# Kernel optimization log

Measured on AMD Instinct MI355X. Metric: run time of the kernel, lower is better.

## Reference

```python
import jax, jax.numpy as jnp
import numpy as np

D_MODEL = 1024
NUM_HEADS = 16
D_K = D_MODEL // NUM_HEADS


def setup_inputs() -> dict:
    key = jax.random.key(0)
    k1, k2, k3, k4, k5 = jax.random.split(key, 5)
    x = jax.random.normal(k1, (2, 2048, D_MODEL), dtype=jnp.float32)
    s = 1.0 / np.sqrt(D_MODEL)
    W_q = jax.random.normal(k2, (D_MODEL, D_MODEL), dtype=jnp.float32) * s
    W_k = jax.random.normal(k3, (D_MODEL, D_MODEL), dtype=jnp.float32) * s
    W_v = jax.random.normal(k4, (D_MODEL, D_MODEL), dtype=jnp.float32) * s
    W_o = jax.random.normal(k5, (D_MODEL, D_MODEL), dtype=jnp.float32) * s
    return {"x": x, "W_q": W_q, "W_k": W_k, "W_v": W_v, "W_o": W_o}


def reference(x, W_q, W_k, W_v, W_o):
    B, S, _ = x.shape
    # projections (nn.Linear: y = x @ W.T); split heads -> (B, H, S, d_k)
    def split_heads(y):
        return y.reshape(B, S, NUM_HEADS, D_K).transpose(0, 2, 1, 3)
    Q = split_heads(x @ W_q.T)
    K = split_heads(x @ W_k.T)
    V = split_heads(x @ W_v.T)
    scale = 1.0 / jnp.sqrt(jnp.asarray(D_K, dtype=x.dtype))
    scores = jnp.einsum("bhqd,bhkd->bhqk", Q, K) * scale  # (B,H,S,S)
    causal = jnp.triu(jnp.ones((S, S), dtype=bool), k=1)
    scores = jnp.where(causal, -jnp.inf, scores)
    attn = jax.nn.softmax(scores, axis=-1)
    out = jnp.einsum("bhqk,bhkd->bhqd", attn, V)
    out = out.transpose(0, 2, 1, 3).reshape(B, S, D_MODEL)
    return out @ W_o.T
```

## Files before the change

### kernel.cpp

```cpp
#include <hip/hip_runtime.h>
#include <hip/hip_bf16.h>

typedef __bf16 bf16x8 __attribute__((ext_vector_type(8)));
typedef float f32x4 __attribute__((ext_vector_type(4)));
typedef float f32x16 __attribute__((ext_vector_type(16)));
typedef unsigned short ushort_t;
typedef unsigned int uint2v __attribute__((ext_vector_type(2)));

#define DEVI __device__ __forceinline__

static constexpr int KDIM = 1024;
static constexpr int SEQ  = 2048;
static constexpr size_t TEN = 4194304;

DEVI ushort_t f2bf(float f) {
  union { float f; unsigned u; } a; a.f = f;
  unsigned u = a.u;
  return (ushort_t)((u + 0x7FFFu + ((u >> 16) & 1u)) >> 16);
}

DEVI unsigned cvtpk(float lo, float hi) {
  unsigned r;
  asm("v_cvt_pk_bf16_f32 %0, %1, %2" : "=v"(r) : "v"(lo), "v"(hi));
  return r;
}

DEVI uint2v plswap(unsigned a, unsigned b) {
  return __builtin_amdgcn_permlane32_swap(a, b, 0, 0);
}
DEVI float swap_max(float x) {
  union { float f; unsigned u; } a; a.f = x;
  const uint2v r = plswap(a.u, a.u);
  union { unsigned u; float f; } p0, p1; p0.u = r[0]; p1.u = r[1];
  return fmaxf(p0.f, p1.f);
}
DEVI float swap_sum(float x) {
  union { float f; unsigned u; } a; a.f = x;
  const uint2v r = plswap(a.u, a.u);
  union { unsigned u; float f; } p0, p1; p0.u = r[0]; p1.u = r[1];
  return p0.f + p1.f;
}

DEVI void gload16(const ushort_t* g, ushort_t* l) {
  __builtin_amdgcn_global_load_lds(
      (const __attribute__((address_space(1))) void*)g,
      (__attribute__((address_space(3))) void*)l,
      16, 0, 0);
}

__global__ void cast_all(const float* __restrict__ x,
                         const float* __restrict__ w0, const float* __restrict__ w1,
                         const float* __restrict__ w2, const float* __restrict__ w3,
                         ushort_t* __restrict__ xb, ushort_t* __restrict__ wb) {
  const int i = blockIdx.x * 256 + threadIdx.x;
  float4 v; ushort_t* dst; int idx;
  if (i < (1 << 20)) {
    v = ((const float4*)x)[i]; dst = xb; idx = i;
  } else {
    const int j = i - (1 << 20);
    const int which = j >> 18;
    const float* w = which == 0 ? w0 : which == 1 ? w1 : which == 2 ? w2 : w3;
    v = ((const float4*)w)[j & 262143]; dst = wb; idx = j;
  }
  ushort4 o;
  o.x = f2bf(v.x); o.y = f2bf(v.y); o.z = f2bf(v.z); o.w = f2bf(v.w);
  ((ushort4*)dst)[idx] = o;
}

template<int MODE>
__global__ __launch_bounds__(256, 3) void gemm128(const ushort_t* __restrict__ A,
                                                  const ushort_t* __restrict__ Bm,
                                                  ushort_t* __restrict__ qfo,
                                                  ushort_t* __restrict__ kfo,
                                                  ushort_t* __restrict__ vfo,
                                                  float* __restrict__ ofp) {
  __shared__ ushort_t smA[128 * 64];
  __shared__ ushort_t smB[128 * 64];
  const int tid = threadIdx.x;
  const int w = tid >> 6, l = tid & 63;
  const int lg = l >> 4, ll = l & 15;
  const int lr = l >> 3, lc = (l & 7) * 8;
  const int m0 = blockIdx.y * 128, n0 = blockIdx.x * 128;
  const int wm = (w >> 1) * 64, wn = (w & 1) * 64;

  f32x4 acc[4][4];
#pragma unroll
  for (int i = 0; i < 4; ++i)
#pragma unroll
    for (int j = 0; j < 4; ++j) acc[i][j] = f32x4{0.f, 0.f, 0.f, 0.f};

  for (int k0 = 0; k0 < KDIM; k0 += 64) {
    __syncthreads();
#pragma unroll
    for (int i = 0; i < 4; ++i) {
      const int ci = w * 4 + i;
      gload16(A  + (size_t)(m0 + ci * 8 + lr) * KDIM + k0 + lc, smA + ci * 512);
      gload16(Bm + (size_t)(n0 + ci * 8 + lr) * KDIM + k0 + lc, smB + ci * 512);
    }
    __syncthreads();
#pragma unroll
    for (int ks = 0; ks < 2; ++ks) {
      bf16x8 af[4], bfr[4];
#pragma unroll
      for (int t = 0; t < 4; ++t) {
        af[t]  = *(const bf16x8*)(smA + (wm + t * 16 + ll) * 64 + ks * 32 + lg * 8);
        bfr[t] = *(const bf16x8*)(smB + (wn + t * 16 + ll) * 64 + ks * 32 + lg * 8);
      }
      __builtin_amdgcn_s_setprio(1);
#pragma unroll
      for (int i = 0; i < 4; ++i)
#pragma unroll
        for (int j = 0; j < 4; ++j)
          acc[i][j] = __builtin_amdgcn_mfma_f32_16x16x32_bf16(af[i], bfr[j], acc[i][j], 0, 0, 0);
      __builtin_amdgcn_s_setprio(0);
    }
  }

#pragma unroll
  for (int i = 0; i < 4; ++i) {
#pragma unroll
    for (int j = 0; j < 4; ++j) {
      const int gm0 = m0 + wm + i * 16 + 4 * lg;
      const int gn = n0 + wn + j * 16 + ll;
      if (MODE == 0) {
        const int which = gn >> 10, nn = gn & 1023;
        const int h = nn >> 6, d = nn & 63;
        const int b = gm0 >> 11, s0 = gm0 & 2047;
        const size_t bh = (size_t)(b * 16 + h);
        if (which == 0) {
          const int ks = d >> 4, hiv = (d >> 3) & 1, j7 = d & 7;
#pragma unroll
          for (int r = 0; r < 4; ++r) {
            const int s = s0 + r;
            qfo[((bh * 64 + (s >> 5)) * 4 + ks) * 512 + (hiv * 32 + (s & 31)) * 8 + j7] =
                f2bf(acc[i][j][r]);
          }
        } else if (which == 1) {
          const int ks = d >> 4, hiv = (d >> 3) & 1, j7 = d & 7;
#pragma unroll
          for (int r = 0; r < 4; ++r) {
            const int s = s0 + r;
            kfo[((bh * 32 + (s >> 6)) * 8 + ((s >> 5) & 1) * 4 + ks) * 512 +
                (hiv * 32 + (s & 31)) * 8 + j7] = f2bf(acc[i][j][r]);
          }
        } else {
          const size_t base = ((bh * 32 + (s0 >> 6)) * 8 + (d >> 5) * 4 + ((s0 >> 4) & 3)) * 512 +
                              (((s0 >> 3) & 1) * 32 + (d & 31)) * 8 + (s0 & 7);
          const unsigned u0 = cvtpk(acc[i][j][0], acc[i][j][1]);
          const unsigned u1 = cvtpk(acc[i][j][2], acc[i][j][3]);
          *(uint2v*)(vfo + base) = uint2v{u0, u1};
        }
      } else {
#pragma unroll
        for (int r = 0; r < 4; ++r)
          ofp[(size_t)(gm0 + r) * 1024 + gn] = acc[i][j][r];
      }
    }
  }
}

__global__ __launch_bounds__(256, 2) void attn_fwd(const ushort_t* __restrict__ Qf,
                                                   const ushort_t* __restrict__ Kf,
                                                   const ushort_t* __restrict__ Vf,
                                                   ushort_t* __restrict__ ao) {
  const int tid = threadIdx.x;
  const int w = tid >> 6, l = tid & 63;
  const int l31 = l & 31, hi = l >> 5;
  const int bh = blockIdx.y;
  const int qx = ((bh >> 4) & 1) ? (15 - (int)blockIdx.x) : (int)blockIdx.x;
  const int q0 = qx * 128;
  const int q = q0 + w * 32 + l31;

  const ushort_t* Qw = Qf + ((size_t)bh * 64 + (q0 >> 5) + w) * 4 * 512 + l * 8;
  const ushort_t* Kb = Kf + (size_t)bh * 32 * 8 * 512 + l * 8;
  const ushort_t* Vb = Vf + (size_t)bh * 32 * 8 * 512 + l * 8;

  bf16x8 qf[4];
#pragma unroll
  for (int ks = 0; ks < 4; ++ks)
    qf[ks] = *(const bf16x8*)(Qw + ks * 512);

  f32x16 oT[2];
#pragma unroll
  for (int dh = 0; dh < 2; ++dh)
#pragma unroll
    for (int r = 0; r < 16; ++r) oT[dh][r] = 0.f;
  float mi = -3.0e38f, li = 0.f;

  const float SCL2 = 0.18033688011112042f;
  const int myNkt = (q0 + 32 * w + 31) / 64 + 1;

  bf16x8 kf[8];
#pragma unroll
  for (int f = 0; f < 8; ++f) kf[f] = *(const bf16x8*)(Kb + f * 512);

  for (int kt = 0; kt < myNkt; ++kt) {
    const ushort_t* Vt_ = Vb + (size_t)kt * 8 * 512;
    bf16x8 vf[8];
#pragma unroll
    for (int f = 0; f < 8; ++f) vf[f] = *(const bf16x8*)(Vt_ + f * 512);

    f32x16 sc[2];
#pragma unroll
    for (int h2 = 0; h2 < 2; ++h2)
#pragma unroll
      for (int r = 0; r < 16; ++r) sc[h2][r] = 0.f;
    __builtin_amdgcn_s_setprio(1);
#pragma unroll
    for (int h2 = 0; h2 < 2; ++h2)
#pragma unroll
      for (int ks = 0; ks < 4; ++ks)
        sc[h2] = __builtin_amdgcn_mfma_f32_32x32x16_bf16(kf[h2 * 4 + ks], qf[ks], sc[h2], 0, 0, 0);
    __builtin_amdgcn_s_setprio(0);

    const bool more = (kt + 1 < myNkt);
    bf16x8 kfn[8];
    if (more) {
      const ushort_t* Kt_ = Kb + (size_t)(kt + 1) * 8 * 512;
#pragma unroll
      for (int f = 0; f < 8; ++f) kfn[f] = *(const bf16x8*)(Kt_ + f * 512);
    }

    if (kt == myNkt - 1) {
      const int thr0 = q - kt * 64 - 4 * hi;
#pragma unroll
      for (int r = 0; r < 16; ++r) {
        const int cr = (r & 3) + 8 * (r >> 2);
        if (cr > thr0)      sc[0][r] = -3.0e38f;
        if (cr > thr0 - 32) sc[1][r] = -3.0e38f;
      }
    }

    float t8[8];
#pragma unroll
    for (int r = 0; r < 8; ++r)
      t8[r] = fmaxf(fmaxf(sc[0][r], sc[0][r + 8]), fmaxf(sc[1][r], sc[1][r + 8]));
    float mx = fmaxf(fmaxf(fmaxf(t8[0], t8[1]), fmaxf(t8[2], t8[3])),
                     fmaxf(fmaxf(t8[4], t8[5]), fmaxf(t8[6], t8[7])));
    mx = swap_max(mx);

    if (!__all(mx <= mi + 44.0f)) {
      const float mnew = fmaxf(mi, mx);
      const float al = __builtin_amdgcn_exp2f((mi - mnew) * SCL2);
      li *= al;
#pragma unroll
      for (int dh = 0; dh < 2; ++dh)
#pragma unroll
        for (int r = 0; r < 16; ++r) oT[dh][r] *= al;
      mi = mnew;
    }

    const float ms = mi * SCL2;
#pragma unroll
    for (int h2 = 0; h2 < 2; ++h2)
#pragma unroll
      for (int r = 0; r < 16; ++r)
        sc[h2][r] = __builtin_amdgcn_exp2f(__builtin_fmaf(sc[h2][r], SCL2, -ms));
    float s8[8];
#pragma unroll
    for (int r = 0; r < 8; ++r)
      s8[r] = (sc[0][r] + sc[0][r + 8]) + (sc[1][r] + sc[1][r + 8]);
    float sum = ((s8[0] + s8[1]) + (s8[2] + s8[3])) + ((s8[4] + s8[5]) + (s8[6] + s8[7]));
    li += swap_sum(sum);

    bf16x8 pf[4];
#pragma unroll
    for (int m = 0; m < 4; ++m) {
      const int H = m >> 1, base = (m & 1) * 8;
      const unsigned a0 = cvtpk(sc[H][base + 0], sc[H][base + 1]);
      const unsigned a1 = cvtpk(sc[H][base + 2], sc[H][base + 3]);
      const unsigned a2 = cvtpk(sc[H][base + 4], sc[H][base + 5]);
      const unsigned a3 = cvtpk(sc[H][base + 6], sc[H][base + 7]);
      const uint2v r02 = plswap(a0, a2);
      const uint2v r13 = plswap(a1, a3);
      union { unsigned u[4]; bf16x8 v; } cv;
      cv.u[0] = r02[0]; cv.u[1] = r13[0]; cv.u[2] = r02[1]; cv.u[3] = r13[1];
      pf[m] = cv.v;
    }

    __builtin_amdgcn_s_setprio(1);
#pragma unroll
    for (int dh = 0; dh < 2; ++dh)
#pragma unroll
      for (int m = 0; m < 4; ++m)
        oT[dh] = __builtin_amdgcn_mfma_f32_32x32x16_bf16(vf[dh * 4 + m], pf[m], oT[dh], 0, 0, 0);
    __builtin_amdgcn_s_setprio(0);

    if (more) {
#pragma unroll
      for (int f = 0; f < 8; ++f) kf[f] = kfn[f];
    }
  }

  const float inv = 1.f / li;
  const int b = bh >> 4, h = bh & 15;
  ushort_t* orow = ao + ((size_t)b * 2048 + q) * 1024 + h * 64;
#pragma unroll
  for (int dh = 0; dh < 2; ++dh)
#pragma unroll
    for (int rg = 0; rg < 4; ++rg) {
      const unsigned u0 = cvtpk(oT[dh][4 * rg + 0] * inv, oT[dh][4 * rg + 1] * inv);
      const unsigned u1 = cvtpk(oT[dh][4 * rg + 2] * inv, oT[dh][4 * rg + 3] * inv);
      *(uint2v*)(orow + dh * 32 + hi * 4 + rg * 8) = uint2v{u0, u1};
    }
}

extern "C" void kernel_launch(void* const* d_in, const int* in_sizes, int n_in,
                              void* d_out, int out_size, void* d_ws, size_t ws_size,
                              hipStream_t stream) {
  (void)in_sizes; (void)n_in; (void)out_size; (void)ws_size;
  const float* x  = (const float*)d_in[0];
  const float* wq = (const float*)d_in[1];
  const float* wk = (const float*)d_in[2];
  const float* wv = (const float*)d_in[3];
  const float* wo = (const float*)d_in[4];

  char* ws = (char*)d_ws;
  ushort_t* xb  = (ushort_t*)ws;
  ushort_t* wb  = (ushort_t*)(ws + (8u  << 20));
  ushort_t* qf  = (ushort_t*)(ws + (16u << 20));
  ushort_t* kf  = (ushort_t*)(ws + (24u << 20));
  ushort_t* vf  = (ushort_t*)(ws + (40u << 20));
  ushort_t* ao  = xb;
  float* out = (float*)d_out;

  cast_all<<<8192, 256, 0, stream>>>(x, wq, wk, wv, wo, xb, wb);
  gemm128<0><<<dim3(24, 32), 256, 0, stream>>>(xb, wb, qf, kf, vf, nullptr);
  attn_fwd  <<<dim3(16, 32), 256, 0, stream>>>(qf, kf, vf, ao);
  gemm128<1><<<dim3(8, 32), 256, 0, stream>>>(ao, wb + 3 * 1048576, nullptr, nullptr, nullptr, out);
}
```

Measured before the change: 176.6 us.

## Replace QKV projection GEMM with 256x256-tile, 8-wave, double-buffered pipelined kernel

The QKV projection now uses a dedicated kernel with 256x256 output tiles and 512 threads. It double-buffers LDS in half-K chunks with asynchronous global-to-LDS loads and an XOR swizzle to avoid bank conflicts, and interleaves staging with the MFMA phases using vmcnt waits and barriers. Blocks are remapped so that consecutive tiles spread across XCDs. The goal is more data reuse per tile and hidden memory latency, at the cost of a grid of only 192 blocks, which is under one wave on 256 CUs.

After: 174.5 us. No clear change (-1.2%).

```diff
diff --git a/kernel.cpp b/kernel.cpp
--- a/kernel.cpp
+++ b/kernel.cpp
@@ -67,13 +67,140 @@
   ((ushort4*)dst)[idx] = o;
 }
 
-template<int MODE>
-__global__ __launch_bounds__(256, 3) void gemm128(const ushort_t* __restrict__ A,
-                                                  const ushort_t* __restrict__ Bm,
-                                                  ushort_t* __restrict__ qfo,
-                                                  ushort_t* __restrict__ kfo,
-                                                  ushort_t* __restrict__ vfo,
-                                                  float* __restrict__ ofp) {
+DEVI void stage_half(const ushort_t* __restrict__ G, int rowbase, int kcol,
+                     ushort_t* lbase, int tid) {
+#pragma unroll
+  for (int rd = 0; rd < 2; ++rd) {
+    const int row = rd * 128 + (tid >> 2), cg = tid & 3;
+    const int gcol = kcol + ((cg ^ ((row >> 1) & 3)) << 3);
+    gload16(G + (size_t)(rowbase + row) * 1024 + gcol, lbase + row * 32 + cg * 8);
+  }
+}
+
+__global__ __launch_bounds__(512, 2) void gemm256_qkv(const ushort_t* __restrict__ A,
+                                                      const ushort_t* __restrict__ Bm,
+                                                      ushort_t* __restrict__ qfo,
+                                                      ushort_t* __restrict__ kfo,
+                                                      ushort_t* __restrict__ vfo) {
+  __shared__ ushort_t sm[2][2][2][8192];
+  const int tid = threadIdx.x;
+  const int wid = tid >> 6, l = tid & 63;
+  const int wm = wid >> 2, wn = wid & 3;
+  const int lg = l >> 4, ll = l & 15;
+  const int orig = blockIdx.x;
+  const int wg = (orig & 7) * 24 + (orig >> 3);
+  const int bx = wg % 12, by = wg / 12;
+  const int m0 = by * 256, n0 = bx * 256;
+
+  f32x4 acc[8][4];
+#pragma unroll
+  for (int i = 0; i < 8; ++i)
+#pragma unroll
+    for (int j = 0; j < 4; ++j) acc[i][j] = f32x4{0.f, 0.f, 0.f, 0.f};
+
+#define STG(T, MAT, KH) do { if ((T) < 16) \
+    stage_half((MAT) ? Bm : A, (MAT) ? n0 : m0, (T) * 64 + (KH) * 32, \
+               &sm[(T) & 1][MAT][KH][0], tid); } while (0)
+#define BARX do { asm volatile("" ::: "memory"); __builtin_amdgcn_s_barrier(); \
+                  asm volatile("" ::: "memory"); } while (0)
+#define PHASE(P, KH, MH, STG_STMT, WAIT_STMT) do {                              \
+    bf16x8 af_[4], bf_[4];                                                      \
+    _Pragma("unroll")                                                           \
+    for (int mr = 0; mr < 4; ++mr) {                                            \
+      const int ra = wm * 128 + ((MH) * 4 + mr) * 16 + ll;                      \
+      af_[mr] = *(const bf16x8*)&sm[P][0][KH][ra * 32 + ((lg ^ ((ra >> 1) & 3)) << 3)]; \
+    }                                                                           \
+    _Pragma("unroll")                                                           \
+    for (int nr = 0; nr < 4; ++nr) {                                            \
+      const int rb = wn * 64 + nr * 16 + ll;                                    \
+      bf_[nr] = *(const bf16x8*)&sm[P][1][KH][rb * 32 + ((lg ^ ((rb >> 1) & 3)) << 3)]; \
+    }                                                                           \
+    STG_STMT;                                                                   \
+    BARX;                                                                       \
+    __builtin_amdgcn_s_setprio(1);                                              \
+    _Pragma("unroll")                                                           \
+    for (int mr = 0; mr < 4; ++mr)                                              \
+      _Pragma("unroll")                                                         \
+      for (int nr = 0; nr < 4; ++nr)                                            \
+        acc[(MH) * 4 + mr][nr] = __builtin_amdgcn_mfma_f32_16x16x32_bf16(       \
+            af_[mr], bf_[nr], acc[(MH) * 4 + mr][nr], 0, 0, 0);                 \
+    __builtin_amdgcn_s_setprio(0);                                              \
+    WAIT_STMT;                                                                  \
+    BARX;                                                                       \
+  } while (0)
+#define WAIT4 asm volatile("s_waitcnt vmcnt(4)" ::: "memory")
+#define WAIT0 asm volatile("s_waitcnt vmcnt(0)" ::: "memory")
+
+  STG(0, 0, 0); STG(0, 1, 0); STG(0, 0, 1); STG(0, 1, 1); STG(1, 0, 0); STG(1, 1, 0);
+  WAIT4;
+  BARX;
+
+  for (int I = 0; I < 7; ++I) {
+    const int T = 2 * I;
+    PHASE(0, 0, 0, STG(T + 1, 0, 1), );
+    PHASE(0, 0, 1, STG(T + 1, 1, 1), );
+    PHASE(0, 1, 0, STG(T + 2, 0, 0), );
+    PHASE(0, 1, 1, STG(T + 2, 1, 0), WAIT4);
+    PHASE(1, 0, 0, STG(T + 2, 0, 1), );
+    PHASE(1, 0, 1, STG(T + 2, 1, 1), );
+    PHASE(1, 1, 0, STG(T + 3, 0, 0), );
+    PHASE(1, 1, 1, STG(T + 3, 1, 0), WAIT4);
+  }
+  PHASE(0, 0, 0, STG(15, 0, 1), );
+  PHASE(0, 0, 1, STG(15, 1, 1), );
+  PHASE(0, 1, 0, , );
+  PHASE(0, 1, 1, , WAIT0);
+  PHASE(1, 0, 0, , );
+  PHASE(1, 0, 1, , );
+  PHASE(1, 1, 0, , );
+  PHASE(1, 1, 1, , );
+
+#undef STG
+#undef PHASE
+#undef WAIT4
+#undef WAIT0
+#undef BARX
+
+#pragma unroll
+  for (int mr = 0; mr < 8; ++mr) {
+#pragma unroll
+    for (int nr = 0; nr < 4; ++nr) {
+      const int gm0 = m0 + wm * 128 + mr * 16 + 4 * lg;
+      const int gn = n0 + wn * 64 + nr * 16 + ll;
+      const int which = gn >> 10, nn = gn & 1023;
+      const int h = nn >> 6, d = nn & 63;
+      const int b = gm0 >> 11, s0 = gm0 & 2047;
+      const size_t bh = (size_t)(b * 16 + h);
+      if (which == 0) {
+        const int ks = d >> 4, hiv = (d >> 3) & 1, j7 = d & 7;
+#pragma unroll
+        for (int r = 0; r < 4; ++r) {
+          const int s = s0 + r;
+          qfo[((bh * 64 + (s >> 5)) * 4 + ks) * 512 + (hiv * 32 + (s & 31)) * 8 + j7] =
+              f2bf(acc[mr][nr][r]);
+        }
+      } else if (which == 1) {
+        const int ks = d >> 4, hiv = (d >> 3) & 1, j7 = d & 7;
+#pragma unroll
+        for (int r = 0; r < 4; ++r) {
+          const int s = s0 + r;
+          kfo[((bh * 32 + (s >> 6)) * 8 + ((s >> 5) & 1) * 4 + ks) * 512 +
+              (hiv * 32 + (s & 31)) * 8 + j7] = f2bf(acc[mr][nr][r]);
+        }
+      } else {
+        const size_t base = ((bh * 32 + (s0 >> 6)) * 8 + (d >> 5) * 4 + ((s0 >> 4) & 3)) * 512 +
+                            (((s0 >> 3) & 1) * 32 + (d & 31)) * 8 + (s0 & 7);
+        const unsigned u0 = cvtpk(acc[mr][nr][0], acc[mr][nr][1]);
+        const unsigned u1 = cvtpk(acc[mr][nr][2], acc[mr][nr][3]);
+        *(uint2v*)(vfo + base) = uint2v{u0, u1};
+      }
+    }
+  }
+}
+
+__global__ __launch_bounds__(256, 3) void gemm_out(const ushort_t* __restrict__ A,
+                                                   const ushort_t* __restrict__ Bm,
+                                                   float* __restrict__ ofp) {
   __shared__ ushort_t smA[128 * 64];
   __shared__ ushort_t smB[128 * 64];
   const int tid = threadIdx.x;
@@ -117,46 +244,15 @@
   }
 
 #pragma unroll
-  for (int i = 0; i < 4; ++i) {
+  for (int i = 0; i < 4; ++i)
 #pragma unroll
     for (int j = 0; j < 4; ++j) {
       const int gm0 = m0 + wm + i * 16 + 4 * lg;
       const int gn = n0 + wn + j * 16 + ll;
-      if (MODE == 0) {
-        const int which = gn >> 10, nn = gn & 1023;
-        const int h = nn >> 6, d = nn & 63;
-        const int b = gm0 >> 11, s0 = gm0 & 2047;
-        const size_t bh = (size_t)(b * 16 + h);
-        if (which == 0) {
-          const int ks = d >> 4, hiv = (d >> 3) & 1, j7 = d & 7;
-#pragma unroll
-          for (int r = 0; r < 4; ++r) {
-            const int s = s0 + r;
-            qfo[((bh * 64 + (s >> 5)) * 4 + ks) * 512 + (hiv * 32 + (s & 31)) * 8 + j7] =
-                f2bf(acc[i][j][r]);
-          }
-        } else if (which == 1) {
-          const int ks = d >> 4, hiv = (d >> 3) & 1, j7 = d & 7;
-#pragma unroll
-          for (int r = 0; r < 4; ++r) {
-            const int s = s0 + r;
-            kfo[((bh * 32 + (s >> 6)) * 8 + ((s >> 5) & 1) * 4 + ks) * 512 +
-                (hiv * 32 + (s & 31)) * 8 + j7] = f2bf(acc[i][j][r]);
-          }
-        } else {
-          const size_t base = ((bh * 32 + (s0 >> 6)) * 8 + (d >> 5) * 4 + ((s0 >> 4) & 3)) * 512 +
-                              (((s0 >> 3) & 1) * 32 + (d & 31)) * 8 + (s0 & 7);
-          const unsigned u0 = cvtpk(acc[i][j][0], acc[i][j][1]);
-          const unsigned u1 = cvtpk(acc[i][j][2], acc[i][j][3]);
-          *(uint2v*)(vfo + base) = uint2v{u0, u1};
-        }
-      } else {
-#pragma unroll
-        for (int r = 0; r < 4; ++r)
-          ofp[(size_t)(gm0 + r) * 1024 + gn] = acc[i][j][r];
-      }
-    }
-  }
+#pragma unroll
+      for (int r = 0; r < 4; ++r)
+        ofp[(size_t)(gm0 + r) * 1024 + gn] = acc[i][j][r];
+    }
 }
 
 __global__ __launch_bounds__(256, 2) void attn_fwd(const ushort_t* __restrict__ Qf,
@@ -324,8 +420,8 @@
   ushort_t* ao  = xb;
   float* out = (float*)d_out;
 
-  cast_all<<<8192, 256, 0, stream>>>(x, wq, wk, wv, wo, xb, wb);
-  gemm128<0><<<dim3(24, 32), 256, 0, stream>>>(xb, wb, qf, kf, vf, nullptr);
-  attn_fwd  <<<dim3(16, 32), 256, 0, stream>>>(qf, kf, vf, ao);
-  gemm128<1><<<dim3(8, 32), 256, 0, stream>>>(ao, wb + 3 * 1048576, nullptr, nullptr, nullptr, out);
-}
+  cast_all   <<<8192, 256, 0, stream>>>(x, wq, wk, wv, wo, xb, wb);
+  gemm256_qkv<<<192, 512, 0, stream>>>(xb, wb, qf, kf, vf);
+  attn_fwd   <<<dim3(16, 32), 256, 0, stream>>>(qf, kf, vf, ao);
+  gemm_out   <<<dim3(8, 32), 256, 0, stream>>>(ao, wb + 3 * 1048576, out);
+}
```
